# Performance work log

Measured on AMD Instinct MI355X. Metric: run time of the kernel, lower is better.

The kernel has to match this reference:

```python
import jax, jax.numpy as jnp
import numpy as np

N_FEAT = 9
D_MODEL = 128
N_HEADS = 4
LN_EPS = 1e-5


def setup_inputs() -> dict:
    key = jax.random.key(0)
    ks = jax.random.split(key, 16)
    d, F = D_MODEL, N_FEAT
    s = 0.02
    return {
        "x": jax.random.normal(ks[0], (8, 256, 16, F), dtype=jnp.float32),
        # per-band Linear(1, d): weight (F, d), bias (F, d)
        "band_W": jax.random.normal(ks[1], (F, d), dtype=jnp.float32) * s,
        "band_b": jax.random.normal(ks[2], (F, d), dtype=jnp.float32) * s,
        "freq_pos": jax.random.normal(ks[3], (1, F, d), dtype=jnp.float32) * s,
        # MultiheadAttention packed in-proj (3d, d) and out-proj (d, d)
        "in_proj_w": jax.random.normal(ks[4], (3 * d, d), dtype=jnp.float32) * s,
        "in_proj_b": jax.random.normal(ks[5], (3 * d,), dtype=jnp.float32) * s,
        "out_proj_w": jax.random.normal(ks[6], (d, d), dtype=jnp.float32) * s,
        "out_proj_b": jax.random.normal(ks[7], (d,), dtype=jnp.float32) * s,
        # gate: Linear(F*d, d)
        "gate_w": jax.random.normal(ks[8], (d, F * d), dtype=jnp.float32) * s,
        "gate_b": jax.random.normal(ks[9], (d,), dtype=jnp.float32) * s,
        # output_proj: Linear(F*d, 2d) -> GELU -> Linear(2d, d) -> LayerNorm(d)
        "proj1_w": jax.random.normal(ks[10], (2 * d, F * d), dtype=jnp.float32) * s,
        "proj1_b": jax.random.normal(ks[11], (2 * d,), dtype=jnp.float32) * s,
        "proj2_w": jax.random.normal(ks[12], (d, 2 * d), dtype=jnp.float32) * s,
        "proj2_b": jax.random.normal(ks[13], (d,), dtype=jnp.float32) * s,
        "ln_g": jnp.ones((d,), dtype=jnp.float32),
        "ln_b": jnp.zeros((d,), dtype=jnp.float32),
    }


def _forward(x, band_W, band_b, freq_pos, in_proj_w, in_proj_b,
             out_proj_w, out_proj_b, gate_w, gate_b,
             proj1_w, proj1_b, proj2_w, proj2_b, ln_g, ln_b):
    B, T, C, F = x.shape
    d, H = D_MODEL, N_HEADS
    dh = d // H
    N = B * T * C
    xf = x.reshape(N, F)
    # per-band Linear(1, d) + positional embedding -> (N, F, d)
    tok = xf[:, :, None] * band_W[None] + band_b[None] + freq_pos
    # packed QKV projection (torch MHA semantics)
    qkv = jnp.einsum('nfd,ed->nfe', tok, in_proj_w) + in_proj_b
    q, k, v = jnp.split(qkv, 3, axis=-1)
    q = q.reshape(N, F, H, dh)
    k = k.reshape(N, F, H, dh)
    v = v.reshape(N, F, H, dh)
    scores = jnp.einsum('nqhd,nkhd->nhqk', q, k) / jnp.sqrt(jnp.float32(dh))
    attn = jax.nn.softmax(scores, axis=-1)
    ctx = jnp.einsum('nhqk,nkhd->nqhd', attn, v).reshape(N, F, d)
    attn_out = ctx @ out_proj_w.T + out_proj_b
    flat = attn_out.reshape(N, F * d)
    gate = jax.nn.sigmoid(flat @ gate_w.T + gate_b)
    h = jax.nn.gelu(flat @ proj1_w.T + proj1_b, approximate=False)
    y = h @ proj2_w.T + proj2_b
    mu = jnp.mean(y, axis=-1, keepdims=True)
    var = jnp.mean(jnp.square(y - mu), axis=-1, keepdims=True)
    y = (y - mu) * jax.lax.rsqrt(var + LN_EPS) * ln_g + ln_b
    out = y * gate
    return out.reshape(B, T, C, d)


def reference(x, band_W, band_b, freq_pos, in_proj_w, in_proj_b,
              out_proj_w, out_proj_b, gate_w, gate_b,
              proj1_w, proj1_b, proj2_w, proj2_b, ln_g, ln_b):
    return _forward(x, band_W, band_b, freq_pos, in_proj_w, in_proj_b,
                    out_proj_w, out_proj_b, gate_w, gate_b,
                    proj1_w, proj1_b, proj2_w, proj2_b, ln_g, ln_b)
```

## Files before the change

kernel.cpp:

```cpp
#include <hip/hip_runtime.h>

namespace {
constexpr int FB = 9;
constexpr int FD = 1152;
constexpr float LN_EPS = 1e-5f;
constexpr int NT = 512;

typedef __attribute__((ext_vector_type(8))) short short8v;
typedef __attribute__((ext_vector_type(4))) float float4v;

constexpr int WSA_F  = 0;
constexpr int WSC_F  = 3456;
constexpr int COEF_F = 6912;
constexpr int BF_F   = 8352;
constexpr int OPA_F  = 8736;
constexpr int P2F_B  = 71808;
constexpr int WTA_B  = 137344;

constexpr int LDS_BYTES = 49920;
constexpr int L_LNP  = 16384;
constexpr int L_GATE = 17408;
constexpr int L_COEF = 43008;
constexpr int L_SX   = 48768;

constexpr int NB_WTA  = 72;
constexpr int NB_BIAS = 384;
constexpr int NB_P2   = 64;

__device__ __forceinline__ unsigned short f2bf(float f) {
    unsigned u = __builtin_bit_cast(unsigned, f);
    u += 0x7FFFu + ((u >> 16) & 1u);
    return (unsigned short)(u >> 16);
}
__device__ __forceinline__ unsigned pkr(float lo, float hi) {
    const unsigned a = __builtin_bit_cast(unsigned, lo) + 0x8000u;
    const unsigned b = __builtin_bit_cast(unsigned, hi) + 0x8000u;
    return __builtin_amdgcn_perm(b, a, 0x07060302u);
}
__device__ __forceinline__ float gelu_f(float v) {
    float z = 0.7978845608f * (v + 0.044715f * v * v * v);
    z = fminf(fmaxf(z, -15.f), 15.f);
    const float e = __expf(2.f * z);
    const float th = (e - 1.f) / (e + 1.f);
    return 0.5f * v * (1.f + th);
}
#define MFMA16x32(a, b, c) __builtin_amdgcn_mfma_f32_16x16x32_bf16(a, b, c, 0, 0, 0)
}

__global__ __launch_bounds__(512)
void precompACO(const float* __restrict__ bW, const float* __restrict__ bb,
                const float* __restrict__ fp, const float* __restrict__ ipw,
                const float* __restrict__ ipb, const float* __restrict__ opw,
                float* __restrict__ ws)
{
    __shared__ float sw[128], sc[128], sAv[128], sCv[128];
    const int f = blockIdx.x, t = threadIdx.x;
    if (t < 128) { sw[t] = bW[f * 128 + t]; sc[t] = bb[f * 128 + t] + fp[f * 128 + t]; }
    __syncthreads();
    if (t < 384) {
        const float* row = ipw + (size_t)t * 128;
        float a = 0.f, c = 0.f;
        for (int k = 0; k < 128; k += 4) {
            const float4 w = *(const float4*)(row + k);
            a += sw[k]*w.x + sw[k+1]*w.y + sw[k+2]*w.z + sw[k+3]*w.w;
            c += sc[k]*w.x + sc[k+1]*w.y + sc[k+2]*w.z + sc[k+3]*w.w;
        }
        const float cb = c + ipb[t];
        ws[WSA_F + f * 384 + t] = a;
        ws[WSC_F + f * 384 + t] = cb;
        if (t >= 256) { sAv[t - 256] = a; sCv[t - 256] = cb; }
    }
    __syncthreads();
    for (int d = t; d < 1024; d += 512) {
        const int r = d >> 7, j = d & 127;
        const int h = r >> 1, which = r & 1;
        const float* src = (which ? sCv : sAv) + h * 32;
        const float* op = opw + (size_t)j * 128 + h * 32;
        float s = 0.f;
        #pragma unroll
        for (int ii = 0; ii < 32; ++ii) s += op[ii] * src[ii];
        const int kk = which ? (9 + f) : f;
        ws[OPA_F + (h * 18 + kk) * 128 + j] = s;
    }
}

__global__ __launch_bounds__(512)
void precompWBP(const float* __restrict__ gw, const float* __restrict__ gb,
                const float* __restrict__ p1w, const float* __restrict__ p1b,
                const float* __restrict__ opb, const float* __restrict__ p2w,
                const float* __restrict__ wsf,
                unsigned short* __restrict__ wta, unsigned short* __restrict__ p2f,
                float* __restrict__ ws)
{
    __shared__ float smem[128 * 73 + 128 * 49];
    const int bid = blockIdx.x, t = threadIdx.x;
    if (bid < NB_WTA) {
        float* s_opaT = smem;
        float* s_winT = smem + 128 * 73;
        const int fq = bid % 9, oct = bid / 9;
        const int e0 = oct * 48;
        for (int i = t; i < 9216; i += 512) {
            const int r = i >> 7, j = i & 127;
            s_opaT[j * 73 + r] = wsf[OPA_F + i];
        }
        for (int i = t; i < 6144; i += 512) {
            const int el = i >> 7, j = i & 127;
            const int e = e0 + el;
            const float* Win = (e < 128) ? gw + (size_t)e * FD : p1w + (size_t)(e - 128) * FD;
            s_winT[j * 49 + el] = Win[fq * 128 + j];
        }
        __syncthreads();
        for (int d = t; d < 3456; d += 512) {
            const int el = d / 72, r = d - el * 72;
            const int e = e0 + el;
            float acc = 0.f;
            #pragma unroll 8
            for (int j = 0; j < 128; ++j)
                acc += s_winT[j * 49 + el] * s_opaT[j * 73 + r];
            const int h = r / 18, kk = r - h * 18;
            const int K = (h * 9 + fq) * 18 + kk;
            const int ks = K >> 5, slot = K & 31;
            const int lane = (e & 15) + 16 * (slot >> 3);
            wta[((size_t)((e >> 4) * 21 + ks) * 64 + lane) * 8 + (slot & 7)] = f2bf(acc);
        }
        if (fq == 0) {
            for (int d = t; d < 48 * 24; d += 512) {
                const int el = d / 24, Kp = 648 + d % 24;
                const int e = e0 + el;
                const int ks = Kp >> 5, slot = Kp & 31;
                const int lane = (e & 15) + 16 * (slot >> 3);
                wta[((size_t)((e >> 4) * 21 + ks) * 64 + lane) * 8 + (slot & 7)] = 0;
            }
        }
    } else if (bid == NB_WTA) {
        if (t >= 324) return;
        const int h = t / 81, r = t % 81, fq = r / 9, fk = r % 9;
        const float* A = wsf + WSA_F;
        const float* C = wsf + WSC_F;
        const float* aq = A + fq * 384 + h * 32;
        const float* ak = A + fk * 384 + 128 + h * 32;
        const float* cq = C + fq * 384 + h * 32;
        const float* ck = C + fk * 384 + 128 + h * 32;
        float s2 = 0.f, s1q = 0.f, s1k = 0.f, s0 = 0.f;
        #pragma unroll
        for (int d = 0; d < 32; ++d) {
            s2  += aq[d] * ak[d];
            s1q += aq[d] * ck[d];
            s1k += cq[d] * ak[d];
            s0  += cq[d] * ck[d];
        }
        const float sc = 0.17677669529663687f;
        float* row = ws + COEF_F + (h * 9 + fq) * 40;
        row[fk]      = s2  * sc;
        row[10 + fk] = s1q * sc;
        row[20 + fk] = s1k * sc;
        row[30 + fk] = s0  * sc;
    } else if (bid < NB_WTA + 1 + NB_BIAS) {
        const int e = bid - NB_WTA - 1;
        const float* Win = (e < 128) ? gw + (size_t)e * FD : p1w + (size_t)(e - 128) * FD;
        float acc = 0.f;
        for (int m = t; m < FD; m += 512) acc += Win[m] * opb[m & 127];
        #pragma unroll
        for (int off = 32; off > 0; off >>= 1) acc += __shfl_xor(acc, off);
        const int lane = t & 63, wid = t >> 6;
        if (lane == 0) smem[wid] = acc;
        __syncthreads();
        if (t == 0) {
            float s = (e < 128) ? gb[e] : p1b[e - 128];
            #pragma unroll
            for (int w = 0; w < 8; ++w) s += smem[w];
            ws[BF_F + e] = s;
        }
    } else {
        const int id = (bid - NB_WTA - 1 - NB_BIAS) * 512 + t;
        const int j = id & 7, lane = (id >> 3) & 63, ks = (id >> 9) & 7, nt = id >> 12;
        const int i = nt * 16 + (lane & 15);
        const int r = ks * 32 + (lane >> 4) * 8 + j;
        p2f[id] = f2bf(p2w[i * 256 + r]);
    }
}

__global__ __launch_bounds__(NT, 4)
void fba_main(const float* __restrict__ x, const float* __restrict__ p2b,
              const float* __restrict__ lng, const float* __restrict__ lnb,
              const float* __restrict__ wsf,
              const unsigned short* __restrict__ p2frag,
              const unsigned short* __restrict__ wta,
              float* __restrict__ out)
{
    __shared__ float4 lds4[LDS_BYTES / 16];
    char* lds = (char*)lds4;
    unsigned short* hfrag = (unsigned short*)lds;
    float* lnp = (float*)(lds + L_LNP);
    unsigned short* gateb = (unsigned short*)(lds + L_GATE);
    float* scoef = (float*)(lds + L_COEF);
    float* sx    = (float*)(lds + L_SX);

    const int t = threadIdx.x, lane = t & 63, wid = t >> 6;
    const int col = lane & 15, rg = lane >> 4;
    const int n0 = blockIdx.x * 32;

    for (int i = t; i < 1440; i += NT) scoef[i] = wsf[COEF_F + i];
    for (int i = t; i < 288;  i += NT) sx[i] = x[(size_t)n0 * FB + i];
    if (t < 128) *(float4*)(lds + 40960 + t * 16) = float4{0.f, 0.f, 0.f, 0.f};
    __syncthreads();

    for (int id = t; id < 1152; id += NT) {
        const int p = id >> 5, g = id & 31;
        const int fq = p % 9;
        const float* cf = scoef + p * 40;
        const float* xg = sx + g * FB;
        const float xq = xg[fq];
        float sc[9];
        float m = -1e30f;
        #pragma unroll
        for (int fk = 0; fk < 9; ++fk) {
            const float xk = xg[fk];
            const float v = (cf[fk] * xk + cf[10 + fk]) * xq + cf[20 + fk] * xk + cf[30 + fk];
            sc[fk] = v;
            m = fmaxf(m, v);
        }
        float sum = 0.f;
        #pragma unroll
        for (int fk = 0; fk < 9; ++fk) { sc[fk] = __expf(sc[fk] - m); sum += sc[fk]; }
        const float inv = 1.f / sum;
        float v[18];
        #pragma unroll
        for (int fk = 0; fk < 9; ++fk) {
            const float a = sc[fk] * inv;
            v[fk]     = a * xg[fk];
            v[9 + fk] = a;
        }
        const int mg = g >> 4, gl = g & 15;
        const int K0 = p * 18;
        #pragma unroll
        for (int qq = 0; qq < 9; ++qq) {
            const int K = K0 + 2 * qq;
            const int ks = K >> 5, slot = K & 31;
            const int row = ks * 2 + mg;
            const int u = gl + 16 * (slot >> 3);
            *(unsigned*)(lds + row * 1024 + u * 16 + (slot & 7) * 2) = pkr(v[2 * qq], v[2 * qq + 1]);
        }
    }
    __syncthreads();

    const int ng = wid;
    float4v acc0[3], acc1[3];
    #pragma unroll
    for (int q = 0; q < 3; ++q) {
        const float b = wsf[BF_F + (ng * 3 + q) * 16 + col];
        acc0[q] = float4v{b, b, b, b};
        acc1[q] = float4v{b, b, b, b};
    }
    const unsigned short* bbase = wta + (size_t)(ng * 3) * 21 * 512 + lane * 8;
    #define BLOAD(ks, q) (*(const short8v*)(bbase + ((size_t)(q) * 21 + (ks)) * 512))
    short8v cur0 = BLOAD(0, 0), cur1 = BLOAD(0, 1), cur2 = BLOAD(0, 2);
    #pragma unroll 4
    for (int ks = 0; ks < 20; ++ks) {
        const short8v nxt0 = BLOAD(ks + 1, 0);
        const short8v nxt1 = BLOAD(ks + 1, 1);
        const short8v nxt2 = BLOAD(ks + 1, 2);
        const short8v a0 = *(const short8v*)(lds + ((ks * 2 + 0) * 64 + lane) * 16);
        const short8v a1 = *(const short8v*)(lds + ((ks * 2 + 1) * 64 + lane) * 16);
        acc0[0] = MFMA16x32(a0, cur0, acc0[0]);
        acc1[0] = MFMA16x32(a1, cur0, acc1[0]);
        acc0[1] = MFMA16x32(a0, cur1, acc0[1]);
        acc1[1] = MFMA16x32(a1, cur1, acc1[1]);
        acc0[2] = MFMA16x32(a0, cur2, acc0[2]);
        acc1[2] = MFMA16x32(a1, cur2, acc1[2]);
        cur0 = nxt0; cur1 = nxt1; cur2 = nxt2;
    }
    {
        const short8v a0 = *(const short8v*)(lds + ((20 * 2 + 0) * 64 + lane) * 16);
        const short8v a1 = *(const short8v*)(lds + ((20 * 2 + 1) * 64 + lane) * 16);
        acc0[0] = MFMA16x32(a0, cur0, acc0[0]);
        acc1[0] = MFMA16x32(a1, cur0, acc1[0]);
        acc0[1] = MFMA16x32(a0, cur1, acc0[1]);
        acc1[1] = MFMA16x32(a1, cur1, acc1[1]);
        acc0[2] = MFMA16x32(a0, cur2, acc0[2]);
        acc1[2] = MFMA16x32(a1, cur2, acc1[2]);
    }
    #undef BLOAD
    __syncthreads();

    #pragma unroll
    for (int q = 0; q < 3; ++q) {
        const int e = (ng * 3 + q) * 16 + col;
        #pragma unroll
        for (int j = 0; j < 4; ++j) {
            #pragma unroll
            for (int mi = 0; mi < 2; ++mi) {
                const float vv = (mi == 0) ? acc0[q][j] : acc1[q][j];
                const int token = mi * 16 + rg * 4 + j;
                if (e < 128) {
                    const float gv = 1.f / (1.f + __expf(-vv));
                    gateb[token * 128 + e] = (unsigned short)(gv * 65535.f + 0.5f);
                } else {
                    const int rr = e - 128;
                    const float hv = gelu_f(vv);
                    hfrag[mi * 4096 + (rr >> 5) * 512 + (rg * 4 + j + 16 * ((rr >> 3) & 3)) * 8 + (rr & 7)] = f2bf(hv);
                }
            }
        }
    }
    __syncthreads();

    {
        const int mm = wid & 1, nh = wid >> 1;
        float4v y[2];
        float lg[2], lb[2];
        #pragma unroll
        for (int nti = 0; nti < 2; ++nti) {
            const int i = (nh * 2 + nti) * 16 + col;
            const float b = p2b[i];
            y[nti] = float4v{b, b, b, b};
            lg[nti] = lng[i];
            lb[nti] = lnb[i];
        }
        #pragma unroll
        for (int ks = 0; ks < 8; ++ks) {
            const short8v ah = *(const short8v*)(hfrag + mm * 4096 + ks * 512 + lane * 8);
            #pragma unroll
            for (int nti = 0; nti < 2; ++nti) {
                const short8v bw = *(const short8v*)(p2frag + (((nh * 2 + nti) * 8 + ks) * 64 + lane) * 8);
                y[nti] = MFMA16x32(ah, bw, y[nti]);
            }
        }
        #pragma unroll
        for (int j = 0; j < 4; ++j) {
            const int token = mm * 16 + rg * 4 + j;
            float s = y[0][j] + y[1][j];
            float qq = y[0][j] * y[0][j] + y[1][j] * y[1][j];
            s  += __shfl_xor(s, 1);  s  += __shfl_xor(s, 2);
            s  += __shfl_xor(s, 4);  s  += __shfl_xor(s, 8);
            qq += __shfl_xor(qq, 1); qq += __shfl_xor(qq, 2);
            qq += __shfl_xor(qq, 4); qq += __shfl_xor(qq, 8);
            if (col == 0) {
                lnp[token * 8 + nh * 2]     = s;
                lnp[token * 8 + nh * 2 + 1] = qq;
            }
        }
        __syncthreads();
        #pragma unroll
        for (int j = 0; j < 4; ++j) {
            const int token = mm * 16 + rg * 4 + j;
            const float s  = lnp[token * 8] + lnp[token * 8 + 2] + lnp[token * 8 + 4] + lnp[token * 8 + 6];
            const float qq = lnp[token * 8 + 1] + lnp[token * 8 + 3] + lnp[token * 8 + 5] + lnp[token * 8 + 7];
            const float mu = s * (1.f / 128.f);
            const float var = qq * (1.f / 128.f) - mu * mu;
            const float inv = rsqrtf(var + LN_EPS);
            float* op = out + (size_t)(n0 + token) * 128;
            #pragma unroll
            for (int nti = 0; nti < 2; ++nti) {
                const int i = (nh * 2 + nti) * 16 + col;
                const float gv = (float)gateb[token * 128 + i] * (1.f / 65535.f);
                op[i] = ((y[nti][j] - mu) * inv * lg[nti] + lb[nti]) * gv;
            }
        }
    }
}

extern "C" void kernel_launch(void* const* d_in, const int* in_sizes, int n_in,
                              void* d_out, int out_size, void* d_ws, size_t ws_size,
                              hipStream_t stream)
{
    const float* x          = (const float*)d_in[0];
    const float* band_W     = (const float*)d_in[1];
    const float* band_b     = (const float*)d_in[2];
    const float* freq_pos   = (const float*)d_in[3];
    const float* in_proj_w  = (const float*)d_in[4];
    const float* in_proj_b  = (const float*)d_in[5];
    const float* out_proj_w = (const float*)d_in[6];
    const float* out_proj_b = (const float*)d_in[7];
    const float* gate_w     = (const float*)d_in[8];
    const float* gate_b     = (const float*)d_in[9];
    const float* proj1_w    = (const float*)d_in[10];
    const float* proj1_b    = (const float*)d_in[11];
    const float* proj2_w    = (const float*)d_in[12];
    const float* proj2_b    = (const float*)d_in[13];
    const float* ln_g       = (const float*)d_in[14];
    const float* ln_b       = (const float*)d_in[15];
    float* outp = (float*)d_out;

    float* wsf = (float*)d_ws;
    unsigned short* p2f = (unsigned short*)((char*)d_ws + P2F_B);
    unsigned short* wta = (unsigned short*)((char*)d_ws + WTA_B);

    const int Ntok = in_sizes[0] / FB;
    const int nblk = Ntok / 32;

    hipLaunchKernelGGL(precompACO, dim3(9), dim3(512), 0, stream,
                       band_W, band_b, freq_pos, in_proj_w, in_proj_b, out_proj_w, wsf);
    hipLaunchKernelGGL(precompWBP, dim3(NB_WTA + 1 + NB_BIAS + NB_P2), dim3(512), 0, stream,
                       gate_w, gate_b, proj1_w, proj1_b, out_proj_b, proj2_w, wsf, wta, p2f, wsf);
    hipLaunchKernelGGL(fba_main,   dim3(nblk), dim3(NT), 0, stream,
                       x, proj2_b, ln_g, ln_b, wsf, p2f, wta, outp);
}
```

Baseline: 74.14 us.

## Rebalance precompute kernels and raise wave priority around MFMA bursts

```diff
diff --git a/kernel.cpp b/kernel.cpp
--- a/kernel.cpp
+++ b/kernel.cpp
@@ -23,9 +23,10 @@
 constexpr int L_COEF = 43008;
 constexpr int L_SX   = 48768;
 
-constexpr int NB_WTA  = 72;
+constexpr int NB_ACO  = 9;
 constexpr int NB_BIAS = 384;
 constexpr int NB_P2   = 64;
+constexpr int NB_WTA  = 72;
 
 __device__ __forceinline__ unsigned short f2bf(float f) {
     unsigned u = __builtin_bit_cast(unsigned, f);
@@ -48,49 +49,78 @@
 }
 
 __global__ __launch_bounds__(512)
-void precompACO(const float* __restrict__ bW, const float* __restrict__ bb,
-                const float* __restrict__ fp, const float* __restrict__ ipw,
-                const float* __restrict__ ipb, const float* __restrict__ opw,
-                float* __restrict__ ws)
+void precompK1(const float* __restrict__ bW, const float* __restrict__ bb,
+               const float* __restrict__ fp, const float* __restrict__ ipw,
+               const float* __restrict__ ipb, const float* __restrict__ opw,
+               const float* __restrict__ gw, const float* __restrict__ gb,
+               const float* __restrict__ p1w, const float* __restrict__ p1b,
+               const float* __restrict__ opb, const float* __restrict__ p2w,
+               unsigned short* __restrict__ p2f, float* __restrict__ ws)
 {
-    __shared__ float sw[128], sc[128], sAv[128], sCv[128];
-    const int f = blockIdx.x, t = threadIdx.x;
-    if (t < 128) { sw[t] = bW[f * 128 + t]; sc[t] = bb[f * 128 + t] + fp[f * 128 + t]; }
-    __syncthreads();
-    if (t < 384) {
-        const float* row = ipw + (size_t)t * 128;
-        float a = 0.f, c = 0.f;
-        for (int k = 0; k < 128; k += 4) {
-            const float4 w = *(const float4*)(row + k);
-            a += sw[k]*w.x + sw[k+1]*w.y + sw[k+2]*w.z + sw[k+3]*w.w;
-            c += sc[k]*w.x + sc[k+1]*w.y + sc[k+2]*w.z + sc[k+3]*w.w;
-        }
-        const float cb = c + ipb[t];
-        ws[WSA_F + f * 384 + t] = a;
-        ws[WSC_F + f * 384 + t] = cb;
-        if (t >= 256) { sAv[t - 256] = a; sCv[t - 256] = cb; }
-    }
-    __syncthreads();
-    for (int d = t; d < 1024; d += 512) {
-        const int r = d >> 7, j = d & 127;
-        const int h = r >> 1, which = r & 1;
-        const float* src = (which ? sCv : sAv) + h * 32;
-        const float* op = opw + (size_t)j * 128 + h * 32;
-        float s = 0.f;
-        #pragma unroll
-        for (int ii = 0; ii < 32; ++ii) s += op[ii] * src[ii];
-        const int kk = which ? (9 + f) : f;
-        ws[OPA_F + (h * 18 + kk) * 128 + j] = s;
+    __shared__ float smem[512];
+    const int bid = blockIdx.x, t = threadIdx.x;
+    if (bid < NB_ACO) {
+        float* sw  = smem;
+        float* sc  = smem + 128;
+        float* sAv = smem + 256;
+        float* sCv = smem + 384;
+        const int f = bid;
+        if (t < 128) { sw[t] = bW[f * 128 + t]; sc[t] = bb[f * 128 + t] + fp[f * 128 + t]; }
+        __syncthreads();
+        if (t < 384) {
+            const float* row = ipw + (size_t)t * 128;
+            float a = 0.f, c = 0.f;
+            for (int k = 0; k < 128; k += 4) {
+                const float4 w = *(const float4*)(row + k);
+                a += sw[k]*w.x + sw[k+1]*w.y + sw[k+2]*w.z + sw[k+3]*w.w;
+                c += sc[k]*w.x + sc[k+1]*w.y + sc[k+2]*w.z + sc[k+3]*w.w;
+            }
+            const float cb = c + ipb[t];
+            ws[WSA_F + f * 384 + t] = a;
+            ws[WSC_F + f * 384 + t] = cb;
+            if (t >= 256) { sAv[t - 256] = a; sCv[t - 256] = cb; }
+        }
+        __syncthreads();
+        for (int d = t; d < 1024; d += 512) {
+            const int r = d >> 7, j = d & 127;
+            const int h = r >> 1, which = r & 1;
+            const float* src = (which ? sCv : sAv) + h * 32;
+            const float* op = opw + (size_t)j * 128 + h * 32;
+            float s = 0.f;
+            #pragma unroll
+            for (int ii = 0; ii < 32; ++ii) s += op[ii] * src[ii];
+            const int kk = which ? (9 + f) : f;
+            ws[OPA_F + (h * 18 + kk) * 128 + j] = s;
+        }
+    } else if (bid < NB_ACO + NB_BIAS) {
+        const int e = bid - NB_ACO;
+        const float* Win = (e < 128) ? gw + (size_t)e * FD : p1w + (size_t)(e - 128) * FD;
+        float acc = 0.f;
+        for (int m = t; m < FD; m += 512) acc += Win[m] * opb[m & 127];
+        #pragma unroll
+        for (int off = 32; off > 0; off >>= 1) acc += __shfl_xor(acc, off);
+        const int lane = t & 63, wid = t >> 6;
+        if (lane == 0) smem[wid] = acc;
+        __syncthreads();
+        if (t == 0) {
+            float s = (e < 128) ? gb[e] : p1b[e - 128];
+            #pragma unroll
+            for (int w = 0; w < 8; ++w) s += smem[w];
+            ws[BF_F + e] = s;
+        }
+    } else {
+        const int id = (bid - NB_ACO - NB_BIAS) * 512 + t;
+        const int j = id & 7, lane = (id >> 3) & 63, ks = (id >> 9) & 7, nt = id >> 12;
+        const int i = nt * 16 + (lane & 15);
+        const int r = ks * 32 + (lane >> 4) * 8 + j;
+        p2f[id] = f2bf(p2w[i * 256 + r]);
     }
 }
 
 __global__ __launch_bounds__(512)
-void precompWBP(const float* __restrict__ gw, const float* __restrict__ gb,
-                const float* __restrict__ p1w, const float* __restrict__ p1b,
-                const float* __restrict__ opb, const float* __restrict__ p2w,
-                const float* __restrict__ wsf,
-                unsigned short* __restrict__ wta, unsigned short* __restrict__ p2f,
-                float* __restrict__ ws)
+void precompK2(const float* __restrict__ gw, const float* __restrict__ p1w,
+               const float* __restrict__ wsf,
+               unsigned short* __restrict__ wta, float* __restrict__ ws)
 {
     __shared__ float smem[128 * 73 + 128 * 49];
     const int bid = blockIdx.x, t = threadIdx.x;
@@ -132,7 +162,7 @@
                 wta[((size_t)((e >> 4) * 21 + ks) * 64 + lane) * 8 + (slot & 7)] = 0;
             }
         }
-    } else if (bid == NB_WTA) {
+    } else {
         if (t >= 324) return;
         const int h = t / 81, r = t % 81, fq = r / 9, fk = r % 9;
         const float* A = wsf + WSA_F;
@@ -155,28 +185,6 @@
         row[10 + fk] = s1q * sc;
         row[20 + fk] = s1k * sc;
         row[30 + fk] = s0  * sc;
-    } else if (bid < NB_WTA + 1 + NB_BIAS) {
-        const int e = bid - NB_WTA - 1;
-        const float* Win = (e < 128) ? gw + (size_t)e * FD : p1w + (size_t)(e - 128) * FD;
-        float acc = 0.f;
-        for (int m = t; m < FD; m += 512) acc += Win[m] * opb[m & 127];
-        #pragma unroll
-        for (int off = 32; off > 0; off >>= 1) acc += __shfl_xor(acc, off);
-        const int lane = t & 63, wid = t >> 6;
-        if (lane == 0) smem[wid] = acc;
-        __syncthreads();
-        if (t == 0) {
-            float s = (e < 128) ? gb[e] : p1b[e - 128];
-            #pragma unroll
-            for (int w = 0; w < 8; ++w) s += smem[w];
-            ws[BF_F + e] = s;
-        }
-    } else {
-        const int id = (bid - NB_WTA - 1 - NB_BIAS) * 512 + t;
-        const int j = id & 7, lane = (id >> 3) & 63, ks = (id >> 9) & 7, nt = id >> 12;
-        const int i = nt * 16 + (lane & 15);
-        const int r = ks * 32 + (lane >> 4) * 8 + j;
-        p2f[id] = f2bf(p2w[i * 256 + r]);
     }
 }
 
@@ -262,23 +270,27 @@
         const short8v nxt2 = BLOAD(ks + 1, 2);
         const short8v a0 = *(const short8v*)(lds + ((ks * 2 + 0) * 64 + lane) * 16);
         const short8v a1 = *(const short8v*)(lds + ((ks * 2 + 1) * 64 + lane) * 16);
+        __builtin_amdgcn_s_setprio(1);
         acc0[0] = MFMA16x32(a0, cur0, acc0[0]);
         acc1[0] = MFMA16x32(a1, cur0, acc1[0]);
         acc0[1] = MFMA16x32(a0, cur1, acc0[1]);
         acc1[1] = MFMA16x32(a1, cur1, acc1[1]);
         acc0[2] = MFMA16x32(a0, cur2, acc0[2]);
         acc1[2] = MFMA16x32(a1, cur2, acc1[2]);
+        __builtin_amdgcn_s_setprio(0);
         cur0 = nxt0; cur1 = nxt1; cur2 = nxt2;
     }
     {
         const short8v a0 = *(const short8v*)(lds + ((20 * 2 + 0) * 64 + lane) * 16);
         const short8v a1 = *(const short8v*)(lds + ((20 * 2 + 1) * 64 + lane) * 16);
+        __builtin_amdgcn_s_setprio(1);
         acc0[0] = MFMA16x32(a0, cur0, acc0[0]);
         acc1[0] = MFMA16x32(a1, cur0, acc1[0]);
         acc0[1] = MFMA16x32(a0, cur1, acc0[1]);
         acc1[1] = MFMA16x32(a1, cur1, acc1[1]);
         acc0[2] = MFMA16x32(a0, cur2, acc0[2]);
         acc1[2] = MFMA16x32(a1, cur2, acc1[2]);
+        __builtin_amdgcn_s_setprio(0);
     }
     #undef BLOAD
     __syncthreads();
@@ -389,10 +401,11 @@
     const int Ntok = in_sizes[0] / FB;
     const int nblk = Ntok / 32;
 
-    hipLaunchKernelGGL(precompACO, dim3(9), dim3(512), 0, stream,
-                       band_W, band_b, freq_pos, in_proj_w, in_proj_b, out_proj_w, wsf);
-    hipLaunchKernelGGL(precompWBP, dim3(NB_WTA + 1 + NB_BIAS + NB_P2), dim3(512), 0, stream,
-                       gate_w, gate_b, proj1_w, proj1_b, out_proj_b, proj2_w, wsf, wta, p2f, wsf);
-    hipLaunchKernelGGL(fba_main,   dim3(nblk), dim3(NT), 0, stream,
+    hipLaunchKernelGGL(precompK1, dim3(NB_ACO + NB_BIAS + NB_P2), dim3(512), 0, stream,
+                       band_W, band_b, freq_pos, in_proj_w, in_proj_b, out_proj_w,
+                       gate_w, gate_b, proj1_w, proj1_b, out_proj_b, proj2_w, p2f, wsf);
+    hipLaunchKernelGGL(precompK2, dim3(NB_WTA + 1), dim3(512), 0, stream,
+                       gate_w, proj1_w, wsf, wta, wsf);
+    hipLaunchKernelGGL(fba_main,  dim3(nblk), dim3(NT), 0, stream,
                        x, proj2_b, ln_g, ln_b, wsf, p2f, wta, outp);
 }
```

After: 71.46 us, median of 2. -3.6%, faster.
